# Performance work log

Hardware: AMD Instinct MI355X
Metric: run time of the kernel (lower is better)

Reference implementation:

```python
import jax, jax.numpy as jnp
import numpy as np

B, S, D, H = 2, 2048, 1024, 16
DH = D // H


def _rel_shift(pos_score):
    # pos_score: [B,H,S,S] -> Transformer-XL relative shift via pad/reshape/slice
    b, h, s1, s2 = pos_score.shape
    zeros = jnp.zeros((b, h, s1, 1), dtype=pos_score.dtype)
    padded = jnp.concatenate([zeros, pos_score], axis=-1)          # [B,H,S1,S2+1]
    padded = padded.reshape(b, h, s2 + 1, s1)                       # [B,H,S2+1,S1]
    return padded[:, :, 1:].reshape(b, h, s1, s2)


def setup_inputs() -> dict:
    key = jax.random.key(0)
    ks = jax.random.split(key, 16)
    sc = 0.02
    return {
        "q": jax.random.normal(ks[0], (B, S, D), jnp.float32),
        "k": jax.random.normal(ks[1], (B, S, D), jnp.float32),
        "v": jax.random.normal(ks[2], (B, S, D), jnp.float32),
        "pos_embedding": jax.random.normal(ks[3], (B, S, D), jnp.float32),
        "Wq": jax.random.normal(ks[4], (D, D), jnp.float32) * sc,
        "bq": jnp.zeros((D,), jnp.float32),
        "Wk": jax.random.normal(ks[5], (D, D), jnp.float32) * sc,
        "bk": jnp.zeros((D,), jnp.float32),
        "Wv": jax.random.normal(ks[6], (D, D), jnp.float32) * sc,
        "bv": jnp.zeros((D,), jnp.float32),
        "Wp": jax.random.normal(ks[7], (D, D), jnp.float32) * sc,
        "u_bias": jax.random.normal(ks[8], (H, DH), jnp.float32) * sc,
        "v_bias": jax.random.normal(ks[9], (H, DH), jnp.float32) * sc,
        "Wo": jax.random.normal(ks[10], (D, D), jnp.float32) * sc,
        "bo": jnp.zeros((D,), jnp.float32),
    }


def reference(q, k, v, pos_embedding, Wq, bq, Wk, bk, Wv, bv, Wp, u_bias, v_bias, Wo, bo):
    b = q.shape[0]
    qh = (q @ Wq.T + bq).reshape(b, -1, H, DH)          # [B,S,H,dh]
    kh = (k @ Wk.T + bk).reshape(b, -1, H, DH)
    vh = (v @ Wv.T + bv).reshape(b, -1, H, DH)
    ph = (pos_embedding @ Wp.T).reshape(b, -1, H, DH)    # pos Linear has no bias
    content = jnp.einsum('bqhd,bkhd->bhqk', qh + u_bias, kh)
    pos = jnp.einsum('bqhd,bkhd->bhqk', qh + v_bias, ph)
    pos = _rel_shift(pos)
    score = (content + pos) / jnp.sqrt(jnp.float32(D))   # scaled by sqrt(d_model), as in source
    attn = jax.nn.softmax(score, axis=-1)                # dropout p=0 -> identity
    out = jnp.einsum('bhqk,bkhd->bqhd', attn, vh).reshape(b, -1, D)
    return out @ Wo.T + bo
```

## Files before the change

kernel.cpp:

```cpp
#include <hip/hip_runtime.h>

#define B_ 2
#define S_ 2048
#define D_ 1024
#define H_ 16
#define DH_ 64

typedef unsigned short u16;
typedef short v8s __attribute__((ext_vector_type(8)));
typedef float v4f __attribute__((ext_vector_type(4)));

__device__ __forceinline__ u16 f2bf(float x) {
    unsigned int u = __float_as_uint(x);
    u += 0x7fffu + ((u >> 16) & 1u);
    return (u16)(u >> 16);
}
__device__ __forceinline__ float bf2f(u16 u) {
    return __uint_as_float(((unsigned int)u) << 16);
}

typedef __attribute__((address_space(1))) void gvoid;
typedef __attribute__((address_space(3))) void lvoid;
#define CP16(g, l) __builtin_amdgcn_global_load_lds((gvoid*)(g), (lvoid*)(l), 16, 0, 0)

__global__ __launch_bounds__(256) void cvt9(
    const float* __restrict__ s0, const float* __restrict__ s1,
    const float* __restrict__ s2, const float* __restrict__ s3,
    const float* __restrict__ s4, const float* __restrict__ s5,
    const float* __restrict__ s6, const float* __restrict__ s7,
    const float* __restrict__ s8,
    u16* __restrict__ d0, u16* __restrict__ d1, u16* __restrict__ d2,
    u16* __restrict__ d3, u16* __restrict__ d4, u16* __restrict__ d5,
    u16* __restrict__ d6, u16* __restrict__ d7, u16* __restrict__ d8,
    int nbig, int nsmall)
{
    int y = blockIdx.y;
    const float* s = y==0?s0:y==1?s1:y==2?s2:y==3?s3:y==4?s4:y==5?s5:y==6?s6:y==7?s7:s8;
    u16* d = y==0?d0:y==1?d1:y==2?d2:y==3?d3:y==4?d4:y==5?d5:y==6?d6:y==7?d7:d8;
    int n4 = (y < 4) ? nbig : nsmall;
    int i = blockIdx.x * 256 + threadIdx.x;
    if (i < n4) {
        float4 v = ((const float4*)s)[i];
        ushort4 o;
        o.x = f2bf(v.x); o.y = f2bf(v.y); o.z = f2bf(v.z); o.w = f2bf(v.w);
        ((ushort4*)d)[i] = o;
    }
}

__global__ __launch_bounds__(256, 3) void gemm_proj(
    const u16* __restrict__ A0, const u16* __restrict__ A1,
    const u16* __restrict__ A2, const u16* __restrict__ A3,
    const u16* __restrict__ W0, const u16* __restrict__ W1,
    const u16* __restrict__ W2, const u16* __restrict__ W3,
    const float* __restrict__ b0, const float* __restrict__ b1,
    const float* __restrict__ b2,
    u16* __restrict__ C0, u16* __restrict__ C1,
    u16* __restrict__ VT, u16* __restrict__ C3)
{
    const int K = D_, N = D_;
    const int proj = blockIdx.z;
    const u16* A = proj==0?A0:proj==1?A1:proj==2?A2:A3;
    const u16* W = proj==0?W0:proj==1?W1:proj==2?W2:W3;
    const float* bias = proj==0?b0:proj==1?b1:proj==2?b2:nullptr;

    __shared__ u16 As[128 * 64];
    __shared__ u16 Ws[128 * 64];
    const int tid  = threadIdx.x;
    const int wave = tid >> 6, lane = tid & 63;
    const int quad = lane >> 4, l15 = lane & 15;
    const int m0 = blockIdx.y * 128, n0 = blockIdx.x * 128;
    const int wr = wave >> 1, wc = wave & 1;

    const int lr8 = lane >> 3;
    const int lc8 = ((lane & 7) ^ lr8) * 8;
    const int ksw = (l15 & 7) * 8;

    v4f acc[4][4];
    #pragma unroll
    for (int i = 0; i < 4; ++i)
        #pragma unroll
        for (int j = 0; j < 4; ++j) acc[i][j] = (v4f){0.f, 0.f, 0.f, 0.f};

    for (int kb = 0; kb < K; kb += 64) {
        __syncthreads();
        #pragma unroll
        for (int c = 0; c < 4; ++c) {
            int seg = wave * 4 + c;
            CP16(A + (size_t)(m0 + seg * 8 + lr8) * K + kb + lc8, &As[seg * 512]);
            CP16(W + (size_t)(n0 + seg * 8 + lr8) * K + kb + lc8, &Ws[seg * 512]);
        }
        __syncthreads();
        #pragma unroll
        for (int kk = 0; kk < 2; ++kk) {
            v8s af[4], bf[4];
            #pragma unroll
            for (int i = 0; i < 4; ++i)
                af[i] = *(const v8s*)&As[(wr * 64 + i * 16 + l15) * 64 + ((kk * 32 + quad * 8) ^ ksw)];
            #pragma unroll
            for (int j = 0; j < 4; ++j)
                bf[j] = *(const v8s*)&Ws[(wc * 64 + j * 16 + l15) * 64 + ((kk * 32 + quad * 8) ^ ksw)];
            #pragma unroll
            for (int i = 0; i < 4; ++i)
                #pragma unroll
                for (int j = 0; j < 4; ++j)
                    acc[i][j] = __builtin_amdgcn_mfma_f32_16x16x32_bf16(af[i], bf[j], acc[i][j], 0, 0, 0);
        }
    }

    float bb[4];
    #pragma unroll
    for (int j = 0; j < 4; ++j)
        bb[j] = bias ? bias[n0 + wc * 64 + j * 16 + l15] : 0.f;

    if (proj == 2) {
        #pragma unroll
        for (int i = 0; i < 4; ++i)
            #pragma unroll
            for (int j = 0; j < 4; ++j) {
                int r0 = m0 + wr * 64 + i * 16 + quad * 4;
                int c  = n0 + wc * 64 + j * 16 + l15;
                ushort4 pw;
                pw.x = f2bf(acc[i][j][0] + bb[j]);
                pw.y = f2bf(acc[i][j][1] + bb[j]);
                pw.z = f2bf(acc[i][j][2] + bb[j]);
                pw.w = f2bf(acc[i][j][3] + bb[j]);
                size_t row_vt = (size_t)((r0 >> 11) * 16 + (c >> 6)) * 64 + (c & 63);
                *(ushort4*)&VT[row_vt * S_ + (r0 & 2047)] = pw;
            }
    } else {
        u16* C = proj == 0 ? C0 : proj == 1 ? C1 : C3;
        #pragma unroll
        for (int i = 0; i < 4; ++i)
            #pragma unroll
            for (int j = 0; j < 4; ++j)
                #pragma unroll
                for (int reg = 0; reg < 4; ++reg) {
                    int r = m0 + wr * 64 + i * 16 + quad * 4 + reg;
                    int c = n0 + wc * 64 + j * 16 + l15;
                    C[(size_t)r * N + c] = f2bf(acc[i][j][reg] + bb[j]);
                }
    }
}

__global__ __launch_bounds__(256, 3) void gemm_out(
    const u16* __restrict__ A, const u16* __restrict__ W,
    const float* __restrict__ bias, float* __restrict__ C)
{
    const int K = D_, N = D_;
    __shared__ u16 As[64 * 64];
    __shared__ u16 Ws[128 * 64];
    const int tid  = threadIdx.x;
    const int wave = tid >> 6, lane = tid & 63;
    const int quad = lane >> 4, l15 = lane & 15;
    const int m0 = blockIdx.y * 64, n0 = blockIdx.x * 128;
    const int wr = wave >> 1, wc = wave & 1;

    const int lr8 = lane >> 3;
    const int lc8 = ((lane & 7) ^ lr8) * 8;
    const int ksw = (l15 & 7) * 8;

    v4f acc[2][4];
    #pragma unroll
    for (int i = 0; i < 2; ++i)
        #pragma unroll
        for (int j = 0; j < 4; ++j) acc[i][j] = (v4f){0.f, 0.f, 0.f, 0.f};

    for (int kb = 0; kb < K; kb += 64) {
        __syncthreads();
        #pragma unroll
        for (int c = 0; c < 2; ++c) {
            int seg = wave * 2 + c;
            CP16(A + (size_t)(m0 + seg * 8 + lr8) * K + kb + lc8, &As[seg * 512]);
        }
        #pragma unroll
        for (int c = 0; c < 4; ++c) {
            int seg = wave * 4 + c;
            CP16(W + (size_t)(n0 + seg * 8 + lr8) * K + kb + lc8, &Ws[seg * 512]);
        }
        __syncthreads();
        #pragma unroll
        for (int kk = 0; kk < 2; ++kk) {
            v8s af[2], bf[4];
            #pragma unroll
            for (int i = 0; i < 2; ++i)
                af[i] = *(const v8s*)&As[(wr * 32 + i * 16 + l15) * 64 + ((kk * 32 + quad * 8) ^ ksw)];
            #pragma unroll
            for (int j = 0; j < 4; ++j)
                bf[j] = *(const v8s*)&Ws[(wc * 64 + j * 16 + l15) * 64 + ((kk * 32 + quad * 8) ^ ksw)];
            #pragma unroll
            for (int i = 0; i < 2; ++i)
                #pragma unroll
                for (int j = 0; j < 4; ++j)
                    acc[i][j] = __builtin_amdgcn_mfma_f32_16x16x32_bf16(af[i], bf[j], acc[i][j], 0, 0, 0);
        }
    }

    #pragma unroll
    for (int i = 0; i < 2; ++i)
        #pragma unroll
        for (int j = 0; j < 4; ++j)
            #pragma unroll
            for (int reg = 0; reg < 4; ++reg) {
                int r = m0 + wr * 32 + i * 16 + quad * 4 + reg;
                int c = n0 + wc * 64 + j * 16 + l15;
                C[(size_t)r * N + c] = acc[i][j][reg] + bias[c];
            }
}

__global__ __launch_bounds__(256)
__attribute__((amdgpu_waves_per_eu(4, 4)))
void rel_attn15(
    const u16* __restrict__ QH, const u16* __restrict__ KH,
    const u16* __restrict__ VT, const u16* __restrict__ PH,
    const float* __restrict__ ub, const float* __restrict__ vb,
    u16* __restrict__ AO)
{
    __shared__ u16 Ks[64 * 64];
    __shared__ u16 VTs[64 * 64];
    __shared__ u16 PmT[4][80][20];
    __shared__ u16 ps[4][16][72];

    const int tid  = threadIdx.x;
    const int wave = tid >> 6, lane = tid & 63;
    const int quad = lane >> 4, l15 = lane & 15;

    const int wg  = blockIdx.x + 32 * blockIdx.y;
    const int xcd = wg & 7;
    const int i2  = wg >> 3;
    const int bh  = xcd + 8 * (i2 & 3);
    const int xt  = i2 >> 2;

    const int q0 = (xt * 4 + wave) * 16;
    const int bb = bh >> 4, h = bh & 15;
    const size_t base = (size_t)bb * S_ * D_ + (size_t)h * DH_;
    const size_t vtb  = (size_t)bh * DH_ * S_;

    const int lr8 = lane >> 3;
    const int lc8 = ((lane & 7) ^ lr8) * 8;
    const int ksw = (l15 & 7) * 8;

    v8s quf[2], qvf0[2], qvf1[2];
    #pragma unroll
    for (int kc = 0; kc < 2; ++kc) {
        int r0 = q0 + l15;
        int r1 = min(r0 + 1, S_ - 1);
        v8s raw0 = *(const v8s*)&QH[base + (size_t)r0 * D_ + kc * 32 + quad * 8];
        v8s raw1 = *(const v8s*)&QH[base + (size_t)r1 * D_ + kc * 32 + quad * 8];
        #pragma unroll
        for (int j = 0; j < 8; ++j) {
            float ubj = ub[h * DH_ + kc * 32 + quad * 8 + j];
            float vbj = vb[h * DH_ + kc * 32 + quad * 8 + j];
            float f0 = bf2f((u16)raw0[j]);
            quf[kc][j]  = (short)f2bf(f0 + ubj);
            qvf0[kc][j] = (short)f2bf(f0 + vbj);
            qvf1[kc][j] = (short)f2bf(bf2f((u16)raw1[j]) + vbj);
        }
    }

    v4f o[4];
    float l_r[4];
    #pragma unroll
    for (int i = 0; i < 4; ++i) { o[i] = (v4f){0.f, 0.f, 0.f, 0.f}; l_r[i] = 0.f; }

    const int wb = l15 - quad * 4 + 15;

    auto body = [&](int k0, const int phase) {
        __syncthreads();

        #pragma unroll
        for (int c = 0; c < 2; ++c) {
            int seg = wave * 2 + c;
            CP16(KH + base + (size_t)(k0 + seg * 8 + lr8) * D_ + lc8, &Ks[seg * 512]);
            CP16(VT + vtb + (size_t)(seg * 8 + lr8) * S_ + k0 + lc8, &VTs[seg * 512]);
        }

        const int tmin = k0 - q0 - 15;
        const int jbase = (phase == 0) ? (S_ - 1 + tmin) : (tmin - 2);

        auto phaddr = [&](int wcl) -> const u16* {
            int rw = wcl * 16 + l15;
            int j;
            if (phase == 1) {
                int t = tmin + rw;
                j = (t <= 0) ? (S_ - 1 + t) : max(t - 2, 0);
            } else {
                j = jbase + rw;
            }
            return &PH[base + (size_t)j * D_ + quad * 8];
        };

        {
            const u16* ph0 = phaddr(0);
            v8s p0 = *(const v8s*)ph0;
            v8s p1 = *(const v8s*)(ph0 + 32);
            const bool doA = (tmin <= 0);
            #pragma unroll
            for (int wcl = 0; wcl < 5; ++wcl) {
                v8s n0, n1;
                if (wcl < 4) {
                    const u16* phn = phaddr(wcl + 1);
                    n0 = *(const v8s*)phn;
                    n1 = *(const v8s*)(phn + 32);
                }
                int rw = wcl * 16 + l15;
                v4f sel;
                if (phase == 1) {
                    int t = tmin + rw;
                    v4f a1 = (v4f){0.f, 0.f, 0.f, 0.f};
                    a1 = __builtin_amdgcn_mfma_f32_16x16x32_bf16(qvf1[0], p0, a1, 0, 0, 0);
                    a1 = __builtin_amdgcn_mfma_f32_16x16x32_bf16(qvf1[1], p1, a1, 0, 0, 0);
                    sel = a1;
                    if (doA) {
                        v4f a0 = (v4f){0.f, 0.f, 0.f, 0.f};
                        a0 = __builtin_amdgcn_mfma_f32_16x16x32_bf16(qvf0[0], p0, a0, 0, 0, 0);
                        a0 = __builtin_amdgcn_mfma_f32_16x16x32_bf16(qvf0[1], p1, a0, 0, 0, 0);
                        sel = (t >= 2) ? a1 : a0;
                    }
                } else {
                    const v8s a0s = (phase == 0) ? qvf0[0] : qvf1[0];
                    const v8s a1s = (phase == 0) ? qvf0[1] : qvf1[1];
                    v4f a = (v4f){0.f, 0.f, 0.f, 0.f};
                    a = __builtin_amdgcn_mfma_f32_16x16x32_bf16(a0s, p0, a, 0, 0, 0);
                    a = __builtin_amdgcn_mfma_f32_16x16x32_bf16(a1s, p1, a, 0, 0, 0);
                    sel = a;
                }
                ushort4 pw;
                pw.x = f2bf(sel[0]); pw.y = f2bf(sel[1]); pw.z = f2bf(sel[2]); pw.w = f2bf(sel[3]);
                *(ushort4*)&PmT[wave][rw][quad * 4] = pw;
                p0 = n0; p1 = n1;
            }
        }

        __syncthreads();

        #pragma unroll
        for (int ct = 0; ct < 4; ++ct) {
            int kr = (ct * 16 + l15) * 64;
            v8s kbf0 = *(const v8s*)&Ks[kr + ((quad * 8) ^ ksw)];
            v8s kbf1 = *(const v8s*)&Ks[kr + ((32 + quad * 8) ^ ksw)];
            v4f cs = (v4f){0.f, 0.f, 0.f, 0.f};
            cs = __builtin_amdgcn_mfma_f32_16x16x32_bf16(quf[0], kbf0, cs, 0, 0, 0);
            cs = __builtin_amdgcn_mfma_f32_16x16x32_bf16(quf[1], kbf1, cs, 0, 0, 0);
            #pragma unroll
            for (int reg = 0; reg < 4; ++reg) {
                int qrow = quad * 4 + reg;
                int wcol = ct * 16 + wb - reg;
                float pos = bf2f(PmT[wave][wcol][qrow]);
                if (phase == 1) {
                    int t = tmin + wcol;
                    if (t == 1) pos = 0.f;
                }
                float e = __expf((cs[reg] + pos) * 0.03125f);
                ps[wave][qrow][ct * 16 + l15] = f2bf(e);
                l_r[reg] += e;
            }
        }

        v8s af0 = *(const v8s*)&ps[wave][l15][quad * 8];
        v8s af1 = *(const v8s*)&ps[wave][l15][32 + quad * 8];
        #pragma unroll
        for (int dt = 0; dt < 4; ++dt) {
            int vr = (dt * 16 + l15) * 64;
            v8s vbf0 = *(const v8s*)&VTs[vr + ((quad * 8) ^ ksw)];
            v8s vbf1 = *(const v8s*)&VTs[vr + ((32 + quad * 8) ^ ksw)];
            o[dt] = __builtin_amdgcn_mfma_f32_16x16x32_bf16(af0, vbf0, o[dt], 0, 0, 0);
            o[dt] = __builtin_amdgcn_mfma_f32_16x16x32_bf16(af1, vbf1, o[dt], 0, 0, 0);
        }
    };

    const int k1end   = (q0 >= 63) ? ((((q0 - 63) >> 6) + 1) << 6) : 0;
    const int k2start = min((((q0 + 80) >> 6) << 6), S_);

    int k0 = 0;
    for (; k0 < k1end; k0 += 64)   body(k0, 0);
    for (; k0 < k2start; k0 += 64) body(k0, 1);
    for (; k0 < S_; k0 += 64)      body(k0, 2);

    #pragma unroll
    for (int reg = 0; reg < 4; ++reg) {
        float s = l_r[reg];
        #pragma unroll
        for (int off = 1; off < 16; off <<= 1)
            s += __shfl_xor(s, off, 16);
        l_r[reg] = 1.f / s;
    }
    #pragma unroll
    for (int dt = 0; dt < 4; ++dt)
        #pragma unroll
        for (int reg = 0; reg < 4; ++reg)
            AO[base + (size_t)(q0 + quad * 4 + reg) * D_ + dt * 16 + l15] =
                f2bf(o[dt][reg] * l_r[reg]);
}

extern "C" void kernel_launch(void* const* d_in, const int* in_sizes, int n_in,
                              void* d_out, int out_size, void* d_ws, size_t ws_size,
                              hipStream_t stream)
{
    (void)in_sizes; (void)n_in; (void)out_size; (void)ws_size;
    const float* q   = (const float*)d_in[0];
    const float* k   = (const float*)d_in[1];
    const float* v   = (const float*)d_in[2];
    const float* pe  = (const float*)d_in[3];
    const float* Wq  = (const float*)d_in[4];
    const float* bq  = (const float*)d_in[5];
    const float* Wk  = (const float*)d_in[6];
    const float* bk  = (const float*)d_in[7];
    const float* Wv  = (const float*)d_in[8];
    const float* bv  = (const float*)d_in[9];
    const float* Wp  = (const float*)d_in[10];
    const float* ub  = (const float*)d_in[11];
    const float* vbs = (const float*)d_in[12];
    const float* Wo  = (const float*)d_in[13];
    const float* bo  = (const float*)d_in[14];
    float* out = (float*)d_out;

    const size_t NSD = (size_t)B_ * S_ * D_;
    const size_t DD  = (size_t)D_ * D_;
    u16* ws = (u16*)d_ws;
    u16* qB  = ws;
    u16* kB  = qB + NSD;
    u16* vB  = kB + NSD;
    u16* pB  = vB + NSD;
    u16* WqB = pB + NSD;
    u16* WkB = WqB + DD;
    u16* WvB = WkB + DD;
    u16* WpB = WvB + DD;
    u16* WoB = WpB + DD;
    u16* QH  = WoB + DD;
    u16* KH  = QH + NSD;
    u16* VT  = KH + NSD;
    u16* PHb = VT + NSD;
    u16* AO  = qB;

    const int M = B_ * S_;

    cvt9<<<dim3((int)(NSD / 4 / 256), 9), 256, 0, stream>>>(
        q, k, v, pe, Wq, Wk, Wv, Wp, Wo,
        qB, kB, vB, pB, WqB, WkB, WvB, WpB, WoB,
        (int)(NSD / 4), (int)(DD / 4));

    gemm_proj<<<dim3(D_ / 128, M / 128, 4), 256, 0, stream>>>(
        qB, kB, vB, pB, WqB, WkB, WvB, WpB, bq, bk, bv, QH, KH, VT, PHb);

    rel_attn15<<<dim3(S_ / 64, B_ * H_), 256, 0, stream>>>(QH, KH, VT, PHb, ub, vbs, AO);

    gemm_out<<<dim3(D_ / 128, M / 64), 256, 0, stream>>>(AO, WoB, bo, out);
}
```

Before: 385.9 us.

## Fuse fp32-to-bf16 activation conversion into projection GEMM A-tile loads

The separate conversion pass now handles only the five weight matrices. The projection GEMM reads the fp32 activations directly, converts them to bf16 in registers and writes them into the swizzled LDS tile. This removes a full write and re-read of four bf16 activation tensors and shrinks the conversion kernel. In exchange, the A-tile loads go through registers instead of the async global-to-LDS path, which raises register pressure and can reduce overlap inside the GEMM. Each A element is also now read as fp32 by all 8 column blocks, doubling the bytes of those repeated reads.

```diff
diff --git a/kernel.cpp b/kernel.cpp
--- a/kernel.cpp
+++ b/kernel.cpp
@@ -23,21 +23,17 @@
 typedef __attribute__((address_space(3))) void lvoid;
 #define CP16(g, l) __builtin_amdgcn_global_load_lds((gvoid*)(g), (lvoid*)(l), 16, 0, 0)
 
-__global__ __launch_bounds__(256) void cvt9(
+__global__ __launch_bounds__(256) void cvt5(
     const float* __restrict__ s0, const float* __restrict__ s1,
     const float* __restrict__ s2, const float* __restrict__ s3,
-    const float* __restrict__ s4, const float* __restrict__ s5,
-    const float* __restrict__ s6, const float* __restrict__ s7,
-    const float* __restrict__ s8,
+    const float* __restrict__ s4,
     u16* __restrict__ d0, u16* __restrict__ d1, u16* __restrict__ d2,
-    u16* __restrict__ d3, u16* __restrict__ d4, u16* __restrict__ d5,
-    u16* __restrict__ d6, u16* __restrict__ d7, u16* __restrict__ d8,
-    int nbig, int nsmall)
+    u16* __restrict__ d3, u16* __restrict__ d4,
+    int n4)
 {
     int y = blockIdx.y;
-    const float* s = y==0?s0:y==1?s1:y==2?s2:y==3?s3:y==4?s4:y==5?s5:y==6?s6:y==7?s7:s8;
-    u16* d = y==0?d0:y==1?d1:y==2?d2:y==3?d3:y==4?d4:y==5?d5:y==6?d6:y==7?d7:d8;
-    int n4 = (y < 4) ? nbig : nsmall;
+    const float* s = y==0?s0:y==1?s1:y==2?s2:y==3?s3:s4;
+    u16* d = y==0?d0:y==1?d1:y==2?d2:y==3?d3:d4;
     int i = blockIdx.x * 256 + threadIdx.x;
     if (i < n4) {
         float4 v = ((const float4*)s)[i];
@@ -48,8 +44,8 @@
 }
 
 __global__ __launch_bounds__(256, 3) void gemm_proj(
-    const u16* __restrict__ A0, const u16* __restrict__ A1,
-    const u16* __restrict__ A2, const u16* __restrict__ A3,
+    const float* __restrict__ A0, const float* __restrict__ A1,
+    const float* __restrict__ A2, const float* __restrict__ A3,
     const u16* __restrict__ W0, const u16* __restrict__ W1,
     const u16* __restrict__ W2, const u16* __restrict__ W3,
     const float* __restrict__ b0, const float* __restrict__ b1,
@@ -59,7 +55,7 @@
 {
     const int K = D_, N = D_;
     const int proj = blockIdx.z;
-    const u16* A = proj==0?A0:proj==1?A1:proj==2?A2:A3;
+    const float* A = proj==0?A0:proj==1?A1:proj==2?A2:A3;
     const u16* W = proj==0?W0:proj==1?W1:proj==2?W2:W3;
     const float* bias = proj==0?b0:proj==1?b1:proj==2?b2:nullptr;
 
@@ -71,9 +67,10 @@
     const int m0 = blockIdx.y * 128, n0 = blockIdx.x * 128;
     const int wr = wave >> 1, wc = wave & 1;
 
-    const int lr8 = lane >> 3;
-    const int lc8 = ((lane & 7) ^ lr8) * 8;
-    const int ksw = (l15 & 7) * 8;
+    const int row8 = lane >> 3;
+    const int k8   = lane & 7;
+    const int lc8  = (k8 ^ row8) * 8;
+    const int ksw  = (l15 & 7) * 8;
 
     v4f acc[4][4];
     #pragma unroll
@@ -82,12 +79,25 @@
         for (int j = 0; j < 4; ++j) acc[i][j] = (v4f){0.f, 0.f, 0.f, 0.f};
 
     for (int kb = 0; kb < K; kb += 64) {
-        __syncthreads();
+        float4 fa[4], fb[4];
         #pragma unroll
         for (int c = 0; c < 4; ++c) {
             int seg = wave * 4 + c;
-            CP16(A + (size_t)(m0 + seg * 8 + lr8) * K + kb + lc8, &As[seg * 512]);
-            CP16(W + (size_t)(n0 + seg * 8 + lr8) * K + kb + lc8, &Ws[seg * 512]);
+            const float* src = A + (size_t)(m0 + seg * 8 + row8) * K + kb + k8 * 8;
+            fa[c] = *(const float4*)src;
+            fb[c] = *(const float4*)(src + 4);
+        }
+        __syncthreads();
+        #pragma unroll
+        for (int c = 0; c < 4; ++c) {
+            int seg = wave * 4 + c;
+            CP16(W + (size_t)(n0 + seg * 8 + row8) * K + kb + lc8, &Ws[seg * 512]);
+            v8s bv;
+            bv[0] = (short)f2bf(fa[c].x); bv[1] = (short)f2bf(fa[c].y);
+            bv[2] = (short)f2bf(fa[c].z); bv[3] = (short)f2bf(fa[c].w);
+            bv[4] = (short)f2bf(fb[c].x); bv[5] = (short)f2bf(fb[c].y);
+            bv[6] = (short)f2bf(fb[c].z); bv[7] = (short)f2bf(fb[c].w);
+            *(v8s*)&As[(seg * 8 + row8) * 64 + ((k8 ^ row8) * 8)] = bv;
         }
         __syncthreads();
         #pragma unroll
@@ -434,13 +444,13 @@
 
     const int M = B_ * S_;
 
-    cvt9<<<dim3((int)(NSD / 4 / 256), 9), 256, 0, stream>>>(
-        q, k, v, pe, Wq, Wk, Wv, Wp, Wo,
-        qB, kB, vB, pB, WqB, WkB, WvB, WpB, WoB,
-        (int)(NSD / 4), (int)(DD / 4));
+    cvt5<<<dim3((int)(DD / 4 / 256), 5), 256, 0, stream>>>(
+        Wq, Wk, Wv, Wp, Wo,
+        WqB, WkB, WvB, WpB, WoB,
+        (int)(DD / 4));
 
     gemm_proj<<<dim3(D_ / 128, M / 128, 4), 256, 0, stream>>>(
-        qB, kB, vB, pB, WqB, WkB, WvB, WpB, bq, bk, bv, QH, KH, VT, PHb);
+        q, k, v, pe, WqB, WkB, WvB, WpB, bq, bk, bv, QH, KH, VT, PHb);
 
     rel_attn15<<<dim3(S_ / 64, B_ * H_), 256, 0, stream>>>(QH, KH, VT, PHb, ub, vbs, AO);
 
```

Result: slower. 403.1 us (+4.5%).
